# Optimization experiments

Hardware: AMD Instinct MI355X
Metric: run time of the kernel (lower is better)

Reference implementation:

```python
import jax, jax.numpy as jnp
import numpy as np

N_HEAD = 16
HEAD_DIM = 64
N_EMBD = N_HEAD * HEAD_DIM  # 1024
B, T = 2, 2048


def _rope(x, cos, sin):
    # x: [B,T,H,D]; cos/sin: [1,T,1,D//2]
    d = x.shape[-1] // 2
    x1, x2 = x[..., :d], x[..., d:]
    y1 = x1 * cos + x2 * sin
    y2 = -x1 * sin + x2 * cos
    return jnp.concatenate([y1, y2], axis=-1).astype(x.dtype)


def _rms_norm(x):
    eps = jnp.finfo(x.dtype).eps
    ms = jnp.mean(jnp.square(x), axis=-1, keepdims=True)
    return x * jax.lax.rsqrt(ms + eps)


def setup_inputs() -> dict:
    key = jax.random.key(0)
    ks = jax.random.split(key, 7)
    s = 1.0 / np.sqrt(N_EMBD)
    return {
        "x": jax.random.normal(ks[0], (B, T, N_EMBD), dtype=jnp.float32),
        "cos": jax.random.uniform(ks[1], (1, T, 1, HEAD_DIM // 2), dtype=jnp.float32),
        "sin": jax.random.uniform(ks[2], (1, T, 1, HEAD_DIM // 2), dtype=jnp.float32),
        "Wq": jax.random.normal(ks[3], (N_EMBD, N_EMBD), dtype=jnp.float32) * s,
        "Wk": jax.random.normal(ks[4], (N_EMBD, N_EMBD), dtype=jnp.float32) * s,
        "Wv": jax.random.normal(ks[5], (N_EMBD, N_EMBD), dtype=jnp.float32) * s,
        "Wo": jax.random.normal(ks[6], (N_EMBD, N_EMBD), dtype=jnp.float32) * s,
    }


def reference(x, cos, sin, Wq, Wk, Wv, Wo):
    Bx, Tx, C = x.shape
    # bias-free linear projections (nn.Linear applies x @ W.T)
    q = (x @ Wq.T).reshape(Bx, Tx, N_HEAD, HEAD_DIM)
    k = (x @ Wk.T).reshape(Bx, Tx, N_HEAD, HEAD_DIM)
    v = (x @ Wv.T).reshape(Bx, Tx, N_HEAD, HEAD_DIM)
    # rotary embedding (T == cos length branch)
    q = _rope(q, cos, sin)
    k = _rope(k, cos, sin)
    # QK RMSNorm (no learned scale)
    q = _rms_norm(q)
    k = _rms_norm(k)
    # non-causal SDPA, scale = 1/sqrt(head_dim)
    scale = 1.0 / np.sqrt(HEAD_DIM)
    scores = jnp.einsum("bthd,bshd->bhts", q, k) * scale
    p = jax.nn.softmax(scores, axis=-1)
    y = jnp.einsum("bhts,bshd->bthd", p, v)
    y = y.reshape(Bx, Tx, C)
    return y @ Wo.T
```

## Files before the change

kernel.cpp:

```cpp
#include <hip/hip_runtime.h>
#include <stdint.h>

typedef __attribute__((ext_vector_type(8))) short short8;
typedef __attribute__((ext_vector_type(4))) float floatx4;

#define B_SZ 2
#define T_SZ 2048
#define NH   16
#define HD   64
#define C_SZ 1024
#define M_SZ (B_SZ * T_SZ)

static __device__ __forceinline__ unsigned int cvt2(float a, float b) {
    unsigned int r;
    asm("v_cvt_pk_bf16_f32 %0, %1, %2" : "=v"(r) : "v"(a), "v"(b));
    return r;
}

static __device__ __forceinline__ void gload_lds16(const void* g, void* l) {
    __builtin_amdgcn_global_load_lds(
        (const __attribute__((address_space(1))) void*)g,
        (__attribute__((address_space(3))) void*)l, 16, 0, 0);
}

__global__ __launch_bounds__(256)
void cvtk(const float* __restrict__ x,
          const float* __restrict__ w0, const float* __restrict__ w1,
          const float* __restrict__ w2, const float* __restrict__ w3,
          unsigned short* __restrict__ xb, unsigned short* __restrict__ wb)
{
    const float* src; unsigned short* dst; int n4;
    const int y = blockIdx.y;
    if (y == 0) { src = x; dst = xb; n4 = (M_SZ * C_SZ) / 4; }
    else {
        src = (y == 1 ? w0 : y == 2 ? w1 : y == 3 ? w2 : w3);
        dst = wb + (size_t)(y - 1) * C_SZ * C_SZ;
        n4 = (C_SZ * C_SZ) / 4;
    }
    for (int i = blockIdx.x * 256 + threadIdx.x; i < n4; i += gridDim.x * 256) {
        float4 f = *(const float4*)&src[(size_t)i * 4];
        uint2 u;
        u.x = cvt2(f.x, f.y);
        u.y = cvt2(f.z, f.w);
        *(uint2*)&dst[(size_t)i * 4] = u;
    }
}

template <int MODE>
__global__ __launch_bounds__(256)
void gemm_nt(const unsigned short* __restrict__ A,
             const unsigned short* __restrict__ Wb,
             const float* __restrict__ cosp,
             const float* __restrict__ sinp,
             unsigned short* __restrict__ qh,
             unsigned short* __restrict__ kh,
             unsigned short* __restrict__ vt,
             float* __restrict__ Cf)
{
    constexpr int K = C_SZ;
    __shared__ __align__(16) unsigned short As[128 * 64];
    __shared__ __align__(16) unsigned short Bs[128 * 64];

    const int tid  = threadIdx.x;
    const int wave = tid >> 6, lane = tid & 63;
    const int wm = wave >> 1, wn = wave & 1;
    const int quad = lane >> 4, l16 = lane & 15;
    const int mb = blockIdx.x * 128, nb = blockIdx.y * 128;
    const int z  = blockIdx.z;

    const unsigned short* Wp = (MODE == 0) ? (Wb + (size_t)z * C_SZ * C_SZ) : Wb;

    floatx4 acc[4][4] = {};

    const int lrow = lane >> 3;
    const int lsw  = lane & 7;

    for (int k0 = 0; k0 < K; k0 += 64) {
        __syncthreads();
        #pragma unroll
        for (int j = 0; j < 4; ++j) {
            int rb = j * 32 + wave * 8;
            int r  = rb + lrow;
            int col = (lsw ^ (r & 7)) * 8;
            gload_lds16(&A[(size_t)(mb + r) * K + k0 + col], &As[rb * 64]);
            gload_lds16(&Wp[(size_t)(nb + r) * K + k0 + col], &Bs[rb * 64]);
        }
        __syncthreads();

        #pragma unroll
        for (int kk = 0; kk < 2; ++kk) {
            short8 af[4], bfr[4];
            #pragma unroll
            for (int mt = 0; mt < 4; ++mt) {
                int r = wm * 64 + mt * 16 + l16;
                af[mt] = *(const short8*)&As[r * 64 + (((kk * 4 + quad) ^ (r & 7)) * 8)];
            }
            #pragma unroll
            for (int nt = 0; nt < 4; ++nt) {
                int r = wn * 64 + nt * 16 + l16;
                bfr[nt] = *(const short8*)&Bs[r * 64 + (((kk * 4 + quad) ^ (r & 7)) * 8)];
            }
            #pragma unroll
            for (int mt = 0; mt < 4; ++mt)
                #pragma unroll
                for (int nt = 0; nt < 4; ++nt)
                    acc[mt][nt] = __builtin_amdgcn_mfma_f32_16x16x32_bf16(
                        af[mt], bfr[nt], acc[mt][nt], 0, 0, 0);
        }
    }

    if (MODE == 1) {
        #pragma unroll
        for (int mt = 0; mt < 4; ++mt)
            #pragma unroll
            for (int nt = 0; nt < 4; ++nt)
                #pragma unroll
                for (int i = 0; i < 4; ++i) {
                    int row = mb + wm * 64 + mt * 16 + quad * 4 + i;
                    int col = nb + wn * 64 + nt * 16 + l16;
                    Cf[(size_t)row * C_SZ + col] = acc[mt][nt][i];
                }
        return;
    }

    const int h = blockIdx.y * 2 + wn;

    if (z == 2) {
        #pragma unroll
        for (int mt = 0; mt < 4; ++mt) {
            int gr0 = mb + wm * 64 + mt * 16 + quad * 4;
            int b = gr0 >> 11, t0 = gr0 & (T_SZ - 1);
            #pragma unroll
            for (int nt = 0; nt < 4; ++nt) {
                int d = nt * 16 + l16;
                uint2 pk;
                pk.x = cvt2(acc[mt][nt][0], acc[mt][nt][1]);
                pk.y = cvt2(acc[mt][nt][2], acc[mt][nt][3]);
                *(uint2*)&vt[((size_t)(b * NH + h) * HD + d) * T_SZ + t0] = pk;
            }
        }
        return;
    }

    unsigned short* dst = (z == 0) ? qh : kh;
    const float qscale = (z == 0) ? (0.125f * 1.4426950408889634f) : 1.0f;
    const float eps = 1.1920929e-07f;

    #pragma unroll
    for (int mt = 0; mt < 4; ++mt) {
        #pragma unroll
        for (int i = 0; i < 4; ++i) {
            int gr = mb + wm * 64 + mt * 16 + quad * 4 + i;
            int b = gr >> 11, t = gr & (T_SZ - 1);
            float ce = cosp[t * 32 + l16];
            float se = sinp[t * 32 + l16];
            float co = cosp[t * 32 + 16 + l16];
            float so = sinp[t * 32 + 16 + l16];
            float a0 = acc[mt][0][i], a1 = acc[mt][1][i];
            float a2 = acc[mt][2][i], a3 = acc[mt][3][i];
            float y0 = a0 * ce + a2 * se;
            float y1 = a1 * co + a3 * so;
            float y2 = a2 * ce - a0 * se;
            float y3 = a3 * co - a1 * so;
            float ss = y0 * y0 + y1 * y1 + y2 * y2 + y3 * y3;
            ss += __shfl_xor(ss, 1, 64);
            ss += __shfl_xor(ss, 2, 64);
            ss += __shfl_xor(ss, 4, 64);
            ss += __shfl_xor(ss, 8, 64);
            float rn = __builtin_amdgcn_rsqf(ss * (1.0f / 64.0f) + eps) * qscale;
            uint2 u;
            u.x = cvt2(y0 * rn, y1 * rn);
            u.y = cvt2(y2 * rn, y3 * rn);
            *(uint2*)&dst[((size_t)(b * NH + h) * T_SZ + t) * HD + l16 * 4] = u;
        }
    }
}

__global__ __launch_bounds__(512, 4)
void attn(const unsigned short* __restrict__ qh,
          const unsigned short* __restrict__ kh,
          const unsigned short* __restrict__ vt,
          unsigned short* __restrict__ yb)
{
    __shared__ __align__(16) char smem[54272];

    const int tid = threadIdx.x;
    const int wave = tid >> 6, lane = tid & 63;
    const int wk = wave & 1, wq = wave >> 1;
    const int quad = lane >> 4, l16 = lane & 15;
    const int qb = blockIdx.x * 128;
    const int h = blockIdx.y, b = blockIdx.z;

    unsigned short* Ps = (unsigned short*)(smem + 32768) + wave * (32 * 40);
    float* lred = (float*)(smem + 53248);
    float* Ored = (float*)smem;

    const unsigned short* Qg = qh + ((size_t)(b * NH + h) * T_SZ + qb) * HD;
    const unsigned short* Kg = kh + (size_t)(b * NH + h) * T_SZ * HD;
    const unsigned short* Vg = vt + (size_t)(b * NH + h) * HD * T_SZ;

    const int srow = wave * 8 + (lane >> 3);
    const int sc   = ((lane & 7) ^ (srow & 7)) * 8;

    gload_lds16(&Kg[(size_t)srow * HD + sc],
                (unsigned short*)(smem) + wave * 512);
    gload_lds16(&Vg[(size_t)srow * T_SZ + 0 + sc],
                (unsigned short*)(smem + 16384) + wave * 512);

    short8 qfr[2][2];
    #pragma unroll
    for (int n = 0; n < 2; ++n)
        #pragma unroll
        for (int c = 0; c < 2; ++c)
            qfr[n][c] = *(const short8*)&Qg[(size_t)(wq * 32 + n * 16 + l16) * HD + c * 32 + quad * 8];

    floatx4 o[4][2] = {};
    float l_acc[2] = {0.f, 0.f};

    for (int it = 0; it < 32; ++it) {
        const int cur = it & 1;
        unsigned short* Ks = (unsigned short*)(smem + cur * 8192);
        unsigned short* Vs = (unsigned short*)(smem + 16384 + cur * 8192);

        __syncthreads();

        {
            const int nst = ((it + 1) & 31) * 64;
            gload_lds16(&Kg[(size_t)(nst + srow) * HD + sc],
                        (unsigned short*)(smem + (cur ^ 1) * 8192) + wave * 512);
            gload_lds16(&Vg[(size_t)srow * T_SZ + nst + sc],
                        (unsigned short*)(smem + 16384 + (cur ^ 1) * 8192) + wave * 512);
        }

        short8 af[2][2];
        #pragma unroll
        for (int kt = 0; kt < 2; ++kt) {
            int r = wk * 32 + kt * 16 + l16;
            #pragma unroll
            for (int cc = 0; cc < 2; ++cc)
                af[kt][cc] = *(const short8*)&Ks[r * 64 + (((cc * 4 + quad) ^ (r & 7)) * 8)];
        }
        short8 av[4];
        #pragma unroll
        for (int nd = 0; nd < 4; ++nd) {
            int r = nd * 16 + l16;
            av[nd] = *(const short8*)&Vs[r * 64 + (((wk * 4 + quad) ^ (r & 7)) * 8)];
        }

        floatx4 s[2][2];
        #pragma unroll
        for (int n = 0; n < 2; ++n) {
            floatx4 z0 = {0.f, 0.f, 0.f, 0.f};
            z0 = __builtin_amdgcn_mfma_f32_16x16x32_bf16(af[0][0], qfr[n][0], z0, 0, 0, 0);
            s[0][n] = __builtin_amdgcn_mfma_f32_16x16x32_bf16(af[0][1], qfr[n][1], z0, 0, 0, 0);
            floatx4 z1 = {0.f, 0.f, 0.f, 0.f};
            z1 = __builtin_amdgcn_mfma_f32_16x16x32_bf16(af[1][0], qfr[n][0], z1, 0, 0, 0);
            s[1][n] = __builtin_amdgcn_mfma_f32_16x16x32_bf16(af[1][1], qfr[n][1], z1, 0, 0, 0);
        }

        #pragma unroll
        for (int kt = 0; kt < 2; ++kt)
            #pragma unroll
            for (int n = 0; n < 2; ++n) {
                float p0 = __builtin_amdgcn_exp2f(s[kt][n][0]);
                float p1 = __builtin_amdgcn_exp2f(s[kt][n][1]);
                float p2 = __builtin_amdgcn_exp2f(s[kt][n][2]);
                float p3 = __builtin_amdgcn_exp2f(s[kt][n][3]);
                l_acc[n] += (p0 + p1) + (p2 + p3);
                uint2 pk;
                pk.x = cvt2(p0, p1);
                pk.y = cvt2(p2, p3);
                *(uint2*)&Ps[(n * 16 + l16) * 40 + kt * 16 + quad * 4] = pk;
            }

        #pragma unroll
        for (int nv = 0; nv < 2; ++nv) {
            short8 pf = *(const short8*)&Ps[(nv * 16 + l16) * 40 + quad * 8];
            #pragma unroll
            for (int nd = 0; nd < 4; ++nd)
                o[nd][nv] = __builtin_amdgcn_mfma_f32_16x16x32_bf16(av[nd], pf, o[nd][nv], 0, 0, 0);
        }
    }

    #pragma unroll
    for (int n = 0; n < 2; ++n) {
        l_acc[n] += __shfl_xor(l_acc[n], 16, 64);
        l_acc[n] += __shfl_xor(l_acc[n], 32, 64);
    }
    if (quad == 0) {
        #pragma unroll
        for (int n = 0; n < 2; ++n)
            lred[wk * 128 + wq * 32 + n * 16 + l16] = l_acc[n];
    }
    __syncthreads();

    if (wk == 1) {
        #pragma unroll
        for (int nv = 0; nv < 2; ++nv)
            #pragma unroll
            for (int nd = 0; nd < 4; ++nd)
                *(floatx4*)&Ored[(size_t)wq * (32 * 68) + (nv * 16 + l16) * 68 + nd * 16 + quad * 4] = o[nd][nv];
    }
    __syncthreads();

    if (wk == 0) {
        #pragma unroll
        for (int nv = 0; nv < 2; ++nv) {
            int qi = wq * 32 + nv * 16 + l16;
            float lt = lred[qi] + lred[128 + qi];
            float inv = 1.0f / lt;
            int t = qb + qi;
            #pragma unroll
            for (int nd = 0; nd < 4; ++nd) {
                floatx4 r = *(const floatx4*)&Ored[(size_t)wq * (32 * 68) + (nv * 16 + l16) * 68 + nd * 16 + quad * 4];
                floatx4 ov = o[nd][nv];
                uint2 u;
                u.x = cvt2((ov[0] + r[0]) * inv, (ov[1] + r[1]) * inv);
                u.y = cvt2((ov[2] + r[2]) * inv, (ov[3] + r[3]) * inv);
                *(uint2*)&yb[((size_t)b * T_SZ + t) * C_SZ + h * 64 + nd * 16 + quad * 4] = u;
            }
        }
    }
}

extern "C" void kernel_launch(void* const* d_in, const int* in_sizes, int n_in,
                              void* d_out, int out_size, void* d_ws, size_t ws_size,
                              hipStream_t stream)
{
    const float* x    = (const float*)d_in[0];
    const float* cosp = (const float*)d_in[1];
    const float* sinp = (const float*)d_in[2];
    const float* Wq   = (const float*)d_in[3];
    const float* Wk   = (const float*)d_in[4];
    const float* Wv   = (const float*)d_in[5];
    const float* Wo   = (const float*)d_in[6];
    float* out = (float*)d_out;

    char* ws = (char*)d_ws;
    unsigned short* xb = (unsigned short*)(ws);
    unsigned short* yb = xb;
    unsigned short* wb = (unsigned short*)(ws + (8u  << 20));
    unsigned short* qh = (unsigned short*)(ws + (16u << 20));
    unsigned short* kh = (unsigned short*)(ws + (24u << 20));
    unsigned short* vt = (unsigned short*)(ws + (32u << 20));

    cvtk<<<dim3(512, 5), 256, 0, stream>>>(x, Wq, Wk, Wv, Wo, xb, wb);
    gemm_nt<0><<<dim3(32, 8, 3), 256, 0, stream>>>(
        xb, wb, cosp, sinp, qh, kh, vt, nullptr);
    attn<<<dim3(16, NH, B_SZ), 512, 0, stream>>>(qh, kh, vt, yb);
    gemm_nt<1><<<dim3(32, 8, 1), 256, 0, stream>>>(
        yb, wb + (size_t)3 * C_SZ * C_SZ, nullptr, nullptr,
        nullptr, nullptr, nullptr, out);
}
```

Baseline: 194.5 us.

## Double-buffer GEMM LDS tiles with K-step 32 to overlap loads and MFMA

```diff
diff --git a/kernel.cpp b/kernel.cpp
--- a/kernel.cpp
+++ b/kernel.cpp
@@ -57,9 +57,8 @@
              unsigned short* __restrict__ vt,
              float* __restrict__ Cf)
 {
-    constexpr int K = C_SZ;
-    __shared__ __align__(16) unsigned short As[128 * 64];
-    __shared__ __align__(16) unsigned short Bs[128 * 64];
+    __shared__ __align__(16) unsigned short As[2][128 * 32];
+    __shared__ __align__(16) unsigned short Bs[2][128 * 32];
 
     const int tid  = threadIdx.x;
     const int wave = tid >> 6, lane = tid & 63;
@@ -72,41 +71,52 @@
 
     floatx4 acc[4][4] = {};
 
-    const int lrow = lane >> 3;
-    const int lsw  = lane & 7;
-
-    for (int k0 = 0; k0 < K; k0 += 64) {
+    const int sr_off = (lane >> 2);
+    const int sslot  = lane & 3;
+
+    #pragma unroll
+    for (int j = 0; j < 2; ++j) {
+        int rb = j * 64 + wave * 16;
+        int r  = rb + sr_off;
+        int col = (sslot ^ ((r >> 1) & 3)) * 8;
+        gload_lds16(&A[(size_t)(mb + r) * C_SZ + col], &As[0][rb * 32]);
+        gload_lds16(&Wp[(size_t)(nb + r) * C_SZ + col], &Bs[0][rb * 32]);
+    }
+
+    for (int kt = 0; kt < 32; ++kt) {
+        const int cur = kt & 1;
+
         __syncthreads();
-        #pragma unroll
-        for (int j = 0; j < 4; ++j) {
-            int rb = j * 32 + wave * 8;
-            int r  = rb + lrow;
-            int col = (lsw ^ (r & 7)) * 8;
-            gload_lds16(&A[(size_t)(mb + r) * K + k0 + col], &As[rb * 64]);
-            gload_lds16(&Wp[(size_t)(nb + r) * K + k0 + col], &Bs[rb * 64]);
-        }
-        __syncthreads();
-
-        #pragma unroll
-        for (int kk = 0; kk < 2; ++kk) {
-            short8 af[4], bfr[4];
-            #pragma unroll
-            for (int mt = 0; mt < 4; ++mt) {
-                int r = wm * 64 + mt * 16 + l16;
-                af[mt] = *(const short8*)&As[r * 64 + (((kk * 4 + quad) ^ (r & 7)) * 8)];
+
+        {
+            const int k0 = ((kt + 1) & 31) * 32;
+            #pragma unroll
+            for (int j = 0; j < 2; ++j) {
+                int rb = j * 64 + wave * 16;
+                int r  = rb + sr_off;
+                int col = k0 + (sslot ^ ((r >> 1) & 3)) * 8;
+                gload_lds16(&A[(size_t)(mb + r) * C_SZ + col], &As[cur ^ 1][rb * 32]);
+                gload_lds16(&Wp[(size_t)(nb + r) * C_SZ + col], &Bs[cur ^ 1][rb * 32]);
             }
-            #pragma unroll
-            for (int nt = 0; nt < 4; ++nt) {
-                int r = wn * 64 + nt * 16 + l16;
-                bfr[nt] = *(const short8*)&Bs[r * 64 + (((kk * 4 + quad) ^ (r & 7)) * 8)];
-            }
-            #pragma unroll
-            for (int mt = 0; mt < 4; ++mt)
-                #pragma unroll
-                for (int nt = 0; nt < 4; ++nt)
-                    acc[mt][nt] = __builtin_amdgcn_mfma_f32_16x16x32_bf16(
-                        af[mt], bfr[nt], acc[mt][nt], 0, 0, 0);
-        }
+        }
+
+        short8 af[4], bfr[4];
+        #pragma unroll
+        for (int mt = 0; mt < 4; ++mt) {
+            int r = wm * 64 + mt * 16 + l16;
+            af[mt] = *(const short8*)&As[cur][r * 32 + ((quad ^ ((r >> 1) & 3)) * 8)];
+        }
+        #pragma unroll
+        for (int nt = 0; nt < 4; ++nt) {
+            int r = wn * 64 + nt * 16 + l16;
+            bfr[nt] = *(const short8*)&Bs[cur][r * 32 + ((quad ^ ((r >> 1) & 3)) * 8)];
+        }
+        #pragma unroll
+        for (int mt = 0; mt < 4; ++mt)
+            #pragma unroll
+            for (int nt = 0; nt < 4; ++nt)
+                acc[mt][nt] = __builtin_amdgcn_mfma_f32_16x16x32_bf16(
+                    af[mt], bfr[nt], acc[mt][nt], 0, 0, 0);
     }
 
     if (MODE == 1) {
```

Result: slower. 202.5 us (+4.1%).
